# Kernel optimization log

Hardware: AMD Instinct MI355X
Metric: run time of the kernel (lower is better)

## Reference

```python
import jax, jax.numpy as jnp
import numpy as np

B, C, S, N, V = 8, 16, 512, 512, 128
EPS = 1e-5

def setup_inputs() -> dict:
    key = jax.random.key(0)
    ks = jax.random.split(key, 9)
    def u(k, shape, scale):
        return jax.random.uniform(k, shape, jnp.float32, -scale, scale)
    attn_scale = 12 * np.sqrt(3.0 / (S * N * V))      # custom attn_init for query / key.left / value2
    xav_vs = np.sqrt(6.0 / (V + S))                    # xavier_uniform for (C, V, S) or (C, S, V)
    xav_nv = np.sqrt(6.0 / (N + V))                    # xavier_uniform for (C, N, V)
    return {
        "x": jax.random.normal(ks[0], (B, C, S, N), jnp.float32),
        "wq": u(ks[1], (C, N, V), attn_scale),          # query weight (other_features=S)
        "k_left": u(ks[2], (C, V, S), attn_scale),      # key left (attn_init)
        "k_right": u(ks[3], (C, N, V), xav_nv),         # key right (xavier)
        "v1_left": u(ks[4], (C, V, S), xav_vs),         # value1 left (xavier, attn_init=False)
        "v1_right": u(ks[5], (C, N, V), attn_scale),    # value1 right (attn_init scale)
        "v2_w": u(ks[6], (C, V, S), attn_scale),        # value2 weight (other_features=N)
        "gamma": jnp.ones((C,), jnp.float32),
        "beta": jnp.zeros((C,), jnp.float32),
    }

def batch_scaler(y, gamma, beta):
    # normalize over dims (0, 2, 3); per-channel affine
    mean = jnp.mean(y, axis=(0, 2, 3), keepdims=True)
    var = jnp.mean(jnp.square(y - mean), axis=(0, 2, 3), keepdims=True)
    yhat = (y - mean) * jax.lax.rsqrt(var + EPS)
    return yhat * gamma[None, :, None, None] + beta[None, :, None, None]

def reference(x, wq, k_left, k_right, v1_left, v1_right, v2_w, gamma, beta):
    # x: [B,C,S,N]
    q = jnp.matmul(x, wq)                               # [B,C,S,V]
    k = jnp.matmul(jnp.matmul(k_left, x), k_right)       # (C,V,S)@x -> [B,C,V,N] @ (C,N,V) -> [B,C,V,V]
    attn = jax.nn.softmax(jnp.einsum('bcsv,bcwv->bcsw', q, k), axis=-1)  # q @ k^T, softmax last dim
    v1 = jnp.matmul(jnp.matmul(v1_left, x), v1_right)    # [B,C,V,V]
    v2 = jnp.matmul(v2_w, x)                             # [B,C,V,N]
    v = jnp.matmul(v1, v2)                               # [B,C,V,N]
    y = x + jnp.matmul(attn, v)                          # [B,C,S,N]
    return batch_scaler(y, gamma, beta)
```

## Files before the change

kernel.cpp:

```cpp
#include <hip/hip_runtime.h>
#include <math.h>


typedef short  bf16x8 __attribute__((ext_vector_type(8)));
typedef short  short8 __attribute__((ext_vector_type(8)));
typedef float  f32x4  __attribute__((ext_vector_type(4)));

__device__ __forceinline__ unsigned short f2bf(float f) {
    union { float f; unsigned u; } v; v.f = f;
    return (unsigned short)((v.u + 0x7FFF + ((v.u >> 16) & 1)) >> 16);
}
__device__ __forceinline__ float bf2f(unsigned short u) {
    union { unsigned u; float f; } v; v.u = (unsigned)u << 16; return v.f;
}

__device__ __forceinline__ void gload16(const void* g, void* l)
{
    __builtin_amdgcn_global_load_lds(
        (const __attribute__((address_space(1))) void*)g,
        (__attribute__((address_space(3))) void*)l, 16, 0, 0);
}

constexpr size_t OB_XB   = 0;
constexpr size_t OB_XT   = OB_XB  + 67108864;
constexpr size_t OB_KLB  = OB_XT  + 67108864;
constexpr size_t OB_V1LB = OB_KLB + 2097152;
constexpr size_t OB_V2WB = OB_V1LB+ 2097152;
constexpr size_t OB_WQT  = OB_V2WB+ 2097152;
constexpr size_t OB_KRT  = OB_WQT + 2097152;
constexpr size_t OB_V1RT = OB_KRT + 2097152;
constexpr size_t OB_BUF  = OB_V1RT+ 2097152;
constexpr size_t OB_V2T  = OB_BUF + 33554432;
constexpr size_t OB_KM   = OB_V2T + 16777216;
constexpr size_t OB_V1M  = OB_KM  + 4194304;
constexpr size_t OB_Q    = OB_V1M + 4194304;
constexpr size_t OB_ATT  = OB_Q   + 16777216;
constexpr size_t OB_VT   = OB_ATT + 16777216;
constexpr size_t OB_ST   = OB_VT  + 16777216;

template<int NSTEPS, int MF, int NF>
__device__ __forceinline__ void mmcore(const char* __restrict__ Ab, int ldaB,
                                       const char* __restrict__ Bb, int ldbB,
                                       f32x4 (&acc)[MF][NF],
                                       char* __restrict__ smA, char* __restrict__ smB,
                                       int wm, int wn)
{
    const int tid = threadIdx.x;
    const int w = tid >> 6, l = tid & 63, g = l >> 4, lr = l & 15;
    const int rl = l >> 3, ch = l & 7;

#pragma unroll 1
    for (int t = 0; t < NSTEPS; ++t) {
#pragma unroll
        for (int j = 0; j < 4; ++j) {
            const int row = w * 32 + j * 8 + rl;
            gload16(Ab + (size_t)row * ldaB + t * 128 + ((ch ^ (row & 7)) * 16),
                    smA + (w * 32 + j * 8) * 128);
        }
#pragma unroll
        for (int j = 0; j < 4; ++j) {
            const int row = w * 32 + j * 8 + rl;
            gload16(Bb + (size_t)row * ldbB + t * 128 + ((ch ^ (row & 7)) * 16),
                    smB + (w * 32 + j * 8) * 128);
        }
        __syncthreads();
#pragma unroll
        for (int ks = 0; ks < 2; ++ks) {
            bf16x8 av[MF], bv[NF];
            const int cc = ks * 4 + g;
#pragma unroll
            for (int i = 0; i < MF; ++i) { int rw = wm + i * 16 + lr;
                av[i] = *(const bf16x8*)(smA + rw * 128 + ((cc ^ (rw & 7)) * 16)); }
#pragma unroll
            for (int j = 0; j < NF; ++j) { int rw = wn + j * 16 + lr;
                bv[j] = *(const bf16x8*)(smB + rw * 128 + ((cc ^ (rw & 7)) * 16)); }
#pragma unroll
            for (int i = 0; i < MF; ++i)
#pragma unroll
                for (int j = 0; j < NF; ++j)
                    acc[i][j] = __builtin_amdgcn_mfma_f32_16x16x32_bf16(av[i], bv[j], acc[i][j], 0, 0, 0);
        }
        __syncthreads();
    }
}

__device__ __forceinline__ void epi_write_rm(const f32x4 (&acc)[4][4], char* sm)
{
    const int tid = threadIdx.x, w = tid >> 6, l = tid & 63, g = l >> 4, lr = l & 15;
    const int wm = (w >> 1) * 64, wn = (w & 1) * 64;
#pragma unroll
    for (int i = 0; i < 4; ++i)
#pragma unroll
        for (int j = 0; j < 4; ++j) {
            const int row = wm + i * 16 + g * 4, col = wn + j * 16 + lr;
#pragma unroll
            for (int r = 0; r < 4; ++r)
                *(unsigned short*)(sm + (row + r) * 272 + col * 2) = f2bf(acc[i][j][r]);
        }
}

__device__ __forceinline__ void epi_write_tr(const f32x4 (&acc)[4][4], char* sm)
{
    const int tid = threadIdx.x, w = tid >> 6, l = tid & 63, g = l >> 4, lr = l & 15;
    const int wm = (w >> 1) * 64, wn = (w & 1) * 64;
#pragma unroll
    for (int i = 0; i < 4; ++i)
#pragma unroll
        for (int j = 0; j < 4; ++j) {
            const int rv = wm + i * 16 + g * 4, cn = wn + j * 16 + lr;
            ushort4 pk = make_ushort4(f2bf(acc[i][j][0]), f2bf(acc[i][j][1]),
                                      f2bf(acc[i][j][2]), f2bf(acc[i][j][3]));
            *(ushort4*)(sm + cn * 272 + rv * 2) = pk;
        }
}

__device__ __forceinline__ void epi_flush(const char* sm, unsigned short* gout, int ldg)
{
    const int tid = threadIdx.x;
    const int r0 = tid >> 4, q = tid & 15;
#pragma unroll
    for (int rep = 0; rep < 8; ++rep) {
        const int row = rep * 16 + r0;
        *(short8*)((short*)gout + (size_t)row * ldg + q * 8) =
            *(const short8*)(sm + row * 272 + q * 16);
    }
    __syncthreads();
}

__global__ __launch_bounds__(256) void k_pre(const float* __restrict__ kl,
                                             const float* __restrict__ v1l,
                                             const float* __restrict__ v2w,
                                             unsigned short* __restrict__ klb,
                                             unsigned short* __restrict__ v1lb,
                                             unsigned short* __restrict__ v2wb,
                                             float* __restrict__ stats)
{
    if (blockIdx.x == 0 && blockIdx.y == 0 && threadIdx.x < 64) stats[threadIdx.x] = 0.f;
    const int sel = blockIdx.y;
    const float* src = sel == 0 ? kl : sel == 1 ? v1l : v2w;
    unsigned short* dst = sel == 0 ? klb : sel == 1 ? v1lb : v2wb;
    for (int i = blockIdx.x * 256 + threadIdx.x; i < 65536; i += gridDim.x * 256) {
        float4 v = ((const float4*)src)[i];
        ((ushort4*)dst)[i] = make_ushort4(f2bf(v.x), f2bf(v.y), f2bf(v.z), f2bf(v.w));
    }
}

__global__ __launch_bounds__(256) void ktransx(const float* __restrict__ x,
                                               unsigned short* __restrict__ xb,
                                               unsigned short* __restrict__ xt)
{
    __shared__ float tl[64][65];
    const int bc = blockIdx.z;
    const int r0 = blockIdx.y * 64, c0 = blockIdx.x * 64;
    const float* src = x + (size_t)bc * 262144;
    const int tid = threadIdx.x, rr = tid >> 4, cc = (tid & 15) * 4;
#pragma unroll
    for (int rep = 0; rep < 4; ++rep) {
        int row = rep * 16 + rr;
        float4 v = *(const float4*)(src + (size_t)(r0 + row) * 512 + c0 + cc);
        *(ushort4*)(xb + (size_t)bc * 262144 + (size_t)(r0 + row) * 512 + c0 + cc) =
            make_ushort4(f2bf(v.x), f2bf(v.y), f2bf(v.z), f2bf(v.w));
        tl[cc + 0][row] = v.x; tl[cc + 1][row] = v.y; tl[cc + 2][row] = v.z; tl[cc + 3][row] = v.w;
    }
    __syncthreads();
#pragma unroll
    for (int rep = 0; rep < 4; ++rep) {
        int crow = rep * 16 + rr;
        *(ushort4*)(xt + (size_t)bc * 262144 + (size_t)(c0 + crow) * 512 + r0 + cc) =
            make_ushort4(f2bf(tl[crow][cc]), f2bf(tl[crow][cc + 1]),
                         f2bf(tl[crow][cc + 2]), f2bf(tl[crow][cc + 3]));
    }
}

__global__ __launch_bounds__(256) void ktransw(const float* __restrict__ wq,
                                               const float* __restrict__ kr,
                                               const float* __restrict__ v1r,
                                               unsigned short* __restrict__ wqt,
                                               unsigned short* __restrict__ krt,
                                               unsigned short* __restrict__ v1rt)
{
    __shared__ float tl[64][65];
    const int p = blockIdx.z, widx = p >> 4, c = p & 15;
    const float* s = (widx == 0 ? wq : widx == 1 ? kr : v1r) + (size_t)c * 65536;
    unsigned short* d = (widx == 0 ? wqt : widx == 1 ? krt : v1rt) + (size_t)c * 65536;
    const int r0 = blockIdx.y * 64, c0 = blockIdx.x * 64;
    const int tid = threadIdx.x, rr = tid >> 4, cc = (tid & 15) * 4;
#pragma unroll
    for (int rep = 0; rep < 4; ++rep) {
        int row = rep * 16 + rr;
        float4 v = *(const float4*)(s + (size_t)(r0 + row) * 128 + c0 + cc);
        tl[cc + 0][row] = v.x; tl[cc + 1][row] = v.y; tl[cc + 2][row] = v.z; tl[cc + 3][row] = v.w;
    }
    __syncthreads();
#pragma unroll
    for (int rep = 0; rep < 4; ++rep) {
        int crow = rep * 16 + rr;
        *(ushort4*)(d + (size_t)(c0 + crow) * 512 + r0 + cc) =
            make_ushort4(f2bf(tl[crow][cc]), f2bf(tl[crow][cc + 1]),
                         f2bf(tl[crow][cc + 2]), f2bf(tl[crow][cc + 3]));
    }
}

__global__ __launch_bounds__(256, 2) void k_wx(const unsigned short* __restrict__ klb,
                                               const unsigned short* __restrict__ v1lb,
                                               const unsigned short* __restrict__ v2wb,
                                               const unsigned short* __restrict__ xt,
                                               unsigned short* __restrict__ bufb,
                                               unsigned short* __restrict__ v2t)
{
    __shared__ char smem[34816];
    char* smA = smem; char* smB = smem + 16384;
    const int mt = blockIdx.x >> 2, n0 = blockIdx.x & 3, bc = blockIdx.y, c = bc & 15;
    const unsigned short* W = mt == 0 ? klb : mt == 1 ? v1lb : v2wb;
    const char* Bb = (const char*)(xt + (size_t)bc * 262144 + (size_t)n0 * 65536);
    const int w = threadIdx.x >> 6;
    f32x4 acc[4][4] = {};
    mmcore<8, 4, 4>((const char*)(W + (size_t)c * 65536), 1024, Bb, 1024, acc, smA, smB,
                    (w >> 1) * 64, (w & 1) * 64);
    if (mt < 2) {
        epi_write_rm(acc, smem);
        __syncthreads();
        epi_flush(smem, bufb + (size_t)bc * 131072 + (size_t)mt * 65536 + n0 * 128, 512);
    } else {
        epi_write_tr(acc, smem);
        __syncthreads();
        epi_flush(smem, v2t + (size_t)bc * 65536 + (size_t)n0 * 16384, 128);
    }
}

__global__ __launch_bounds__(256, 2) void k_kr(const unsigned short* __restrict__ bufb,
                                               const unsigned short* __restrict__ krt,
                                               const unsigned short* __restrict__ v1rt,
                                               unsigned short* __restrict__ kmat,
                                               unsigned short* __restrict__ v1m)
{
    __shared__ char smem[34816];
    char* smA = smem; char* smB = smem + 16384;
    const int mt = blockIdx.x, bc = blockIdx.y, c = bc & 15;
    const int w = threadIdx.x >> 6;
    f32x4 acc[4][4] = {};
    mmcore<8, 4, 4>((const char*)(bufb + (size_t)bc * 131072 + (size_t)mt * 65536), 1024,
                    (const char*)((mt ? v1rt : krt) + (size_t)c * 65536), 1024, acc, smA, smB,
                    (w >> 1) * 64, (w & 1) * 64);
    epi_write_rm(acc, smem);
    __syncthreads();
    epi_flush(smem, (mt ? v1m : kmat) + (size_t)bc * 16384, 128);
}

__global__ __launch_bounds__(256, 2) void k_q(const unsigned short* __restrict__ xb,
                                              const unsigned short* __restrict__ wqt,
                                              unsigned short* __restrict__ q)
{
    __shared__ char smem[34816];
    char* smA = smem; char* smB = smem + 16384;
    const int mt = blockIdx.x, bc = blockIdx.y, c = bc & 15;
    const int w = threadIdx.x >> 6;
    f32x4 acc[4][4] = {};
    mmcore<8, 4, 4>((const char*)(xb + (size_t)bc * 262144 + (size_t)mt * 65536), 1024,
                    (const char*)(wqt + (size_t)c * 65536), 1024, acc, smA, smB,
                    (w >> 1) * 64, (w & 1) * 64);
    epi_write_rm(acc, smem);
    __syncthreads();
    epi_flush(smem, q + (size_t)bc * 65536 + (size_t)mt * 16384, 128);
}

__global__ __launch_bounds__(256, 2) void k_at(const unsigned short* __restrict__ q,
                                               const unsigned short* __restrict__ kmat,
                                               unsigned short* __restrict__ attn)
{
    __shared__ char smem[34816];
    char* smA = smem; char* smB = smem + 16384;
    const int mt = blockIdx.x, bc = blockIdx.y;
    const int tid = threadIdx.x, w = tid >> 6, l = tid & 63, g = l >> 4, lr = l & 15;
    f32x4 acc[2][8] = {};
    mmcore<2, 2, 8>((const char*)(q + (size_t)bc * 65536 + (size_t)mt * 16384), 256,
                    (const char*)(kmat + (size_t)bc * 16384), 256, acc, smA, smB,
                    w * 32, 0);
    char* wsl = smem + w * 8704;
    unsigned short* ob = attn + (size_t)bc * 65536 + (size_t)(mt * 128 + w * 32) * 128;
#pragma unroll
    for (int i = 0; i < 2; ++i)
#pragma unroll
        for (int r = 0; r < 4; ++r) {
            float mx = -3e38f;
#pragma unroll
            for (int fj = 0; fj < 8; ++fj) mx = fmaxf(mx, acc[i][fj][r]);
#pragma unroll
            for (int d = 1; d < 16; d <<= 1) mx = fmaxf(mx, __shfl_xor(mx, d));
            float s = 0.f, e[8];
#pragma unroll
            for (int fj = 0; fj < 8; ++fj) { e[fj] = __expf(acc[i][fj][r] - mx); s += e[fj]; }
#pragma unroll
            for (int d = 1; d < 16; d <<= 1) s += __shfl_xor(s, d);
            const float inv = 1.f / s;
            const int rowh = i * 16 + g * 4 + r;
#pragma unroll
            for (int fj = 0; fj < 8; ++fj)
                *(unsigned short*)(wsl + rowh * 272 + (fj * 16 + lr) * 2) = f2bf(e[fj] * inv);
        }
#pragma unroll
    for (int rep = 0; rep < 8; ++rep) {
        const int row = rep * 4 + (l >> 4);
        *(short8*)((short*)ob + (size_t)row * 128 + (l & 15) * 8) =
            *(const short8*)(wsl + row * 272 + (l & 15) * 16);
    }
}

__global__ __launch_bounds__(256, 2) void k_v(const unsigned short* __restrict__ v2t,
                                              const unsigned short* __restrict__ v1m,
                                              unsigned short* __restrict__ vt)
{
    __shared__ char smem[34816];
    char* smA = smem; char* smB = smem + 16384;
    const int mt = blockIdx.x, bc = blockIdx.y;
    const int w = threadIdx.x >> 6;
    f32x4 acc[4][4] = {};
    mmcore<2, 4, 4>((const char*)(v2t + (size_t)bc * 65536 + (size_t)mt * 16384), 256,
                    (const char*)(v1m + (size_t)bc * 16384), 256, acc, smA, smB,
                    (w >> 1) * 64, (w & 1) * 64);
    epi_write_rm(acc, smem);
    __syncthreads();
    epi_flush(smem, vt + (size_t)bc * 65536 + (size_t)mt * 16384, 128);
}

__global__ __launch_bounds__(256, 2) void k_y(const unsigned short* __restrict__ attn,
                                              const unsigned short* __restrict__ vt,
                                              const float* __restrict__ x,
                                              unsigned short* __restrict__ yb,
                                              float* __restrict__ stats)
{
    __shared__ char smem[34816];
    __shared__ float r1[4], r2[4];
    char* smA = smem; char* smB = smem + 16384;
    const int nx = blockIdx.x, my = blockIdx.y, bc = blockIdx.z, c = bc & 15;
    const int tid = threadIdx.x, w = tid >> 6, l = tid & 63, g = l >> 4, lr = l & 15;
    f32x4 acc[4][4] = {};
    mmcore<2, 4, 4>((const char*)(attn + (size_t)bc * 65536 + (size_t)my * 16384), 256,
                    (const char*)(vt + (size_t)bc * 65536 + (size_t)nx * 16384), 256, acc, smA, smB,
                    (w >> 1) * 64, (w & 1) * 64);
    const float* xw = x + (size_t)bc * 262144 + (size_t)my * 128 * 512 + nx * 128;
    const int wm = (w >> 1) * 64, wn = (w & 1) * 64;
    float lsum = 0.f, lss = 0.f;
#pragma unroll
    for (int i = 0; i < 4; ++i)
#pragma unroll
        for (int j = 0; j < 4; ++j)
#pragma unroll
            for (int r = 0; r < 4; ++r) {
                const int row = wm + i * 16 + g * 4 + r, col = wn + j * 16 + lr;
                const float yv = acc[i][j][r] + xw[(size_t)row * 512 + col];
                lsum += yv; lss += yv * yv;
                *(unsigned short*)(smem + row * 272 + col * 2) = f2bf(yv);
            }
#pragma unroll
    for (int d = 32; d >= 1; d >>= 1) { lsum += __shfl_xor(lsum, d); lss += __shfl_xor(lss, d); }
    if (l == 0) { r1[w] = lsum; r2[w] = lss; }
    __syncthreads();
    epi_flush(smem, yb + (size_t)bc * 262144 + (size_t)my * 128 * 512 + nx * 128, 512);
    if (tid == 0) {
        atomicAdd(&stats[c * 2 + 0], r1[0] + r1[1] + r1[2] + r1[3]);
        atomicAdd(&stats[c * 2 + 1], r2[0] + r2[1] + r2[2] + r2[3]);
    }
}

__global__ void k_fin(float* __restrict__ stats, const float* __restrict__ gamma,
                      const float* __restrict__ beta)
{
    const int c = threadIdx.x;
    if (c < 16) {
        const float cnt  = 2097152.f;
        const float mean = stats[c * 2 + 0] / cnt;
        const float var  = stats[c * 2 + 1] / cnt - mean * mean;
        const float sc   = rsqrtf(var + 1e-5f) * gamma[c];
        stats[32 + c * 2 + 0] = sc;
        stats[32 + c * 2 + 1] = beta[c] - mean * sc;
    }
}

__global__ __launch_bounds__(256) void k_norm(const unsigned short* __restrict__ yb,
                                              float* __restrict__ out,
                                              const float* __restrict__ stats)
{
    const int tot = 4194304;
    for (int i = blockIdx.x * 256 + threadIdx.x; i < tot; i += gridDim.x * 256) {
        const long e = (long)i * 8;
        const int c = (int)(e >> 18) & 15;
        const float sc = stats[32 + c * 2 + 0];
        const float sh = stats[32 + c * 2 + 1];
        short8 v = ((const short8*)yb)[i];
        float4 o0, o1;
        o0.x = bf2f((unsigned short)v[0]) * sc + sh;
        o0.y = bf2f((unsigned short)v[1]) * sc + sh;
        o0.z = bf2f((unsigned short)v[2]) * sc + sh;
        o0.w = bf2f((unsigned short)v[3]) * sc + sh;
        o1.x = bf2f((unsigned short)v[4]) * sc + sh;
        o1.y = bf2f((unsigned short)v[5]) * sc + sh;
        o1.z = bf2f((unsigned short)v[6]) * sc + sh;
        o1.w = bf2f((unsigned short)v[7]) * sc + sh;
        ((float4*)out)[(size_t)i * 2 + 0] = o0;
        ((float4*)out)[(size_t)i * 2 + 1] = o1;
    }
}

extern "C" void kernel_launch(void* const* d_in, const int* in_sizes, int n_in,
                              void* d_out, int out_size, void* d_ws, size_t ws_size,
                              hipStream_t stream)
{
    (void)in_sizes; (void)n_in; (void)out_size; (void)ws_size;
    const float* x     = (const float*)d_in[0];
    const float* wq    = (const float*)d_in[1];
    const float* kl    = (const float*)d_in[2];
    const float* kr    = (const float*)d_in[3];
    const float* v1l   = (const float*)d_in[4];
    const float* v1r   = (const float*)d_in[5];
    const float* v2w   = (const float*)d_in[6];
    const float* gamma = (const float*)d_in[7];
    const float* beta  = (const float*)d_in[8];
    float* out = (float*)d_out;
    char*  ws  = (char*)d_ws;

    unsigned short* xb   = (unsigned short*)(ws + OB_XB);
    unsigned short* yb   = xb;
    unsigned short* xt   = (unsigned short*)(ws + OB_XT);
    unsigned short* klb  = (unsigned short*)(ws + OB_KLB);
    unsigned short* v1lb = (unsigned short*)(ws + OB_V1LB);
    unsigned short* v2wb = (unsigned short*)(ws + OB_V2WB);
    unsigned short* wqt  = (unsigned short*)(ws + OB_WQT);
    unsigned short* krt  = (unsigned short*)(ws + OB_KRT);
    unsigned short* v1rt = (unsigned short*)(ws + OB_V1RT);
    unsigned short* bufb = (unsigned short*)(ws + OB_BUF);
    unsigned short* v2t  = (unsigned short*)(ws + OB_V2T);
    unsigned short* kmat = (unsigned short*)(ws + OB_KM);
    unsigned short* v1m  = (unsigned short*)(ws + OB_V1M);
    unsigned short* q    = (unsigned short*)(ws + OB_Q);
    unsigned short* attn = (unsigned short*)(ws + OB_ATT);
    unsigned short* vt   = (unsigned short*)(ws + OB_VT);
    float*          st   = (float*)(ws + OB_ST);

    hipLaunchKernelGGL(k_pre,   dim3(64, 3),     dim3(256), 0, stream, kl, v1l, v2w, klb, v1lb, v2wb, st);
    hipLaunchKernelGGL(ktransx, dim3(8, 8, 128), dim3(256), 0, stream, x, xb, xt);
    hipLaunchKernelGGL(ktransw, dim3(2, 8, 48),  dim3(256), 0, stream, wq, kr, v1r, wqt, krt, v1rt);
    hipLaunchKernelGGL(k_wx,    dim3(12, 128),   dim3(256), 0, stream, klb, v1lb, v2wb, xt, bufb, v2t);
    hipLaunchKernelGGL(k_kr,    dim3(2, 128),    dim3(256), 0, stream, bufb, krt, v1rt, kmat, v1m);
    hipLaunchKernelGGL(k_q,     dim3(4, 128),    dim3(256), 0, stream, xb, wqt, q);
    hipLaunchKernelGGL(k_at,    dim3(4, 128),    dim3(256), 0, stream, q, kmat, attn);
    hipLaunchKernelGGL(k_v,     dim3(4, 128),    dim3(256), 0, stream, v2t, v1m, vt);
    hipLaunchKernelGGL(k_y,     dim3(4, 4, 128), dim3(256), 0, stream, attn, vt, x, yb, st);
    hipLaunchKernelGGL(k_fin,   dim3(1), dim3(64), 0, stream, st, gamma, beta);
    hipLaunchKernelGGL(k_norm,  dim3(2048),      dim3(256), 0, stream, yb, out, st);
}
```

Before: 251.5 us.

## Fuse Q projection into attention-score kernel and merge small prep kernels

Q is no longer written to global memory. The k_qat kernel computes each 128-row Q tile with MFMA, stores it swizzled in LDS as bf16, and immediately multiplies it against the K matrix and applies the softmax. The weight bf16 conversion and transpose kernels are merged into one launch, and the stats finalize is folded into each k_norm block, which removes three launches in total. The cost is 64KB of LDS per block in k_qat, which may reduce occupancy below the declared 2 blocks per CU, and every norm block now redundantly recomputes the per-channel scale and shift.

```diff
diff --git a/kernel.cpp b/kernel.cpp
--- a/kernel.cpp
+++ b/kernel.cpp
@@ -33,8 +33,7 @@
 constexpr size_t OB_V2T  = OB_BUF + 33554432;
 constexpr size_t OB_KM   = OB_V2T + 16777216;
 constexpr size_t OB_V1M  = OB_KM  + 4194304;
-constexpr size_t OB_Q    = OB_V1M + 4194304;
-constexpr size_t OB_ATT  = OB_Q   + 16777216;
+constexpr size_t OB_ATT  = OB_V1M + 4194304;
 constexpr size_t OB_VT   = OB_ATT + 16777216;
 constexpr size_t OB_ST   = OB_VT  + 16777216;
 
@@ -127,21 +126,55 @@
     __syncthreads();
 }
 
-__global__ __launch_bounds__(256) void k_pre(const float* __restrict__ kl,
-                                             const float* __restrict__ v1l,
-                                             const float* __restrict__ v2w,
-                                             unsigned short* __restrict__ klb,
-                                             unsigned short* __restrict__ v1lb,
-                                             unsigned short* __restrict__ v2wb,
-                                             float* __restrict__ stats)
-{
-    if (blockIdx.x == 0 && blockIdx.y == 0 && threadIdx.x < 64) stats[threadIdx.x] = 0.f;
-    const int sel = blockIdx.y;
-    const float* src = sel == 0 ? kl : sel == 1 ? v1l : v2w;
-    unsigned short* dst = sel == 0 ? klb : sel == 1 ? v1lb : v2wb;
-    for (int i = blockIdx.x * 256 + threadIdx.x; i < 65536; i += gridDim.x * 256) {
-        float4 v = ((const float4*)src)[i];
-        ((ushort4*)dst)[i] = make_ushort4(f2bf(v.x), f2bf(v.y), f2bf(v.z), f2bf(v.w));
+__global__ __launch_bounds__(256) void k_prep(const float* __restrict__ kl,
+                                              const float* __restrict__ v1l,
+                                              const float* __restrict__ v2w,
+                                              const float* __restrict__ wq,
+                                              const float* __restrict__ kr,
+                                              const float* __restrict__ v1r,
+                                              unsigned short* __restrict__ klb,
+                                              unsigned short* __restrict__ v1lb,
+                                              unsigned short* __restrict__ v2wb,
+                                              unsigned short* __restrict__ wqt,
+                                              unsigned short* __restrict__ krt,
+                                              unsigned short* __restrict__ v1rt,
+                                              float* __restrict__ stats)
+{
+    __shared__ float tl[64][65];
+    const int id = blockIdx.x, tid = threadIdx.x;
+    if (id == 0 && tid < 64) stats[tid] = 0.f;
+    if (id < 192) {
+        const int sel = id >> 6, blk = id & 63;
+        const float* src = sel == 0 ? kl : sel == 1 ? v1l : v2w;
+        unsigned short* dst = sel == 0 ? klb : sel == 1 ? v1lb : v2wb;
+#pragma unroll
+        for (int r = 0; r < 4; ++r) {
+            const int i = blk * 1024 + r * 256 + tid;
+            float4 v = ((const float4*)src)[i];
+            ((ushort4*)dst)[i] = make_ushort4(f2bf(v.x), f2bf(v.y), f2bf(v.z), f2bf(v.w));
+        }
+        return;
+    }
+    const int id2 = id - 192;
+    const int p = id2 >> 4, rem = id2 & 15, by = rem >> 1, bx = rem & 1;
+    const int widx = p >> 4, c = p & 15;
+    const float* s = (widx == 0 ? wq : widx == 1 ? kr : v1r) + (size_t)c * 65536;
+    unsigned short* d = (widx == 0 ? wqt : widx == 1 ? krt : v1rt) + (size_t)c * 65536;
+    const int r0 = by * 64, c0 = bx * 64;
+    const int rr = tid >> 4, cc = (tid & 15) * 4;
+#pragma unroll
+    for (int rep = 0; rep < 4; ++rep) {
+        int row = rep * 16 + rr;
+        float4 v = *(const float4*)(s + (size_t)(r0 + row) * 128 + c0 + cc);
+        tl[cc + 0][row] = v.x; tl[cc + 1][row] = v.y; tl[cc + 2][row] = v.z; tl[cc + 3][row] = v.w;
+    }
+    __syncthreads();
+#pragma unroll
+    for (int rep = 0; rep < 4; ++rep) {
+        int crow = rep * 16 + rr;
+        *(ushort4*)(d + (size_t)(c0 + crow) * 512 + r0 + cc) =
+            make_ushort4(f2bf(tl[crow][cc]), f2bf(tl[crow][cc + 1]),
+                         f2bf(tl[crow][cc + 2]), f2bf(tl[crow][cc + 3]));
     }
 }
 
@@ -167,35 +200,6 @@
     for (int rep = 0; rep < 4; ++rep) {
         int crow = rep * 16 + rr;
         *(ushort4*)(xt + (size_t)bc * 262144 + (size_t)(c0 + crow) * 512 + r0 + cc) =
-            make_ushort4(f2bf(tl[crow][cc]), f2bf(tl[crow][cc + 1]),
-                         f2bf(tl[crow][cc + 2]), f2bf(tl[crow][cc + 3]));
-    }
-}
-
-__global__ __launch_bounds__(256) void ktransw(const float* __restrict__ wq,
-                                               const float* __restrict__ kr,
-                                               const float* __restrict__ v1r,
-                                               unsigned short* __restrict__ wqt,
-                                               unsigned short* __restrict__ krt,
-                                               unsigned short* __restrict__ v1rt)
-{
-    __shared__ float tl[64][65];
-    const int p = blockIdx.z, widx = p >> 4, c = p & 15;
-    const float* s = (widx == 0 ? wq : widx == 1 ? kr : v1r) + (size_t)c * 65536;
-    unsigned short* d = (widx == 0 ? wqt : widx == 1 ? krt : v1rt) + (size_t)c * 65536;
-    const int r0 = blockIdx.y * 64, c0 = blockIdx.x * 64;
-    const int tid = threadIdx.x, rr = tid >> 4, cc = (tid & 15) * 4;
-#pragma unroll
-    for (int rep = 0; rep < 4; ++rep) {
-        int row = rep * 16 + rr;
-        float4 v = *(const float4*)(s + (size_t)(r0 + row) * 128 + c0 + cc);
-        tl[cc + 0][row] = v.x; tl[cc + 1][row] = v.y; tl[cc + 2][row] = v.z; tl[cc + 3][row] = v.w;
-    }
-    __syncthreads();
-#pragma unroll
-    for (int rep = 0; rep < 4; ++rep) {
-        int crow = rep * 16 + rr;
-        *(ushort4*)(d + (size_t)(c0 + crow) * 512 + r0 + cc) =
             make_ushort4(f2bf(tl[crow][cc]), f2bf(tl[crow][cc + 1]),
                          f2bf(tl[crow][cc + 2]), f2bf(tl[crow][cc + 3]));
     }
@@ -247,35 +251,73 @@
     epi_flush(smem, (mt ? v1m : kmat) + (size_t)bc * 16384, 128);
 }
 
-__global__ __launch_bounds__(256, 2) void k_q(const unsigned short* __restrict__ xb,
-                                              const unsigned short* __restrict__ wqt,
-                                              unsigned short* __restrict__ q)
-{
-    __shared__ char smem[34816];
-    char* smA = smem; char* smB = smem + 16384;
+__global__ __launch_bounds__(256, 2) void k_qat(const unsigned short* __restrict__ xb,
+                                                const unsigned short* __restrict__ wqt,
+                                                const unsigned short* __restrict__ kmat,
+                                                unsigned short* __restrict__ attn)
+{
+    __shared__ char smem[65536];
+    char* smA = smem;
+    char* smB = smem + 16384;
+    char* qlds = smem + 32768;
     const int mt = blockIdx.x, bc = blockIdx.y, c = bc & 15;
-    const int w = threadIdx.x >> 6;
+    const int tid = threadIdx.x, w = tid >> 6, l = tid & 63, g = l >> 4, lr = l & 15;
+
     f32x4 acc[4][4] = {};
     mmcore<8, 4, 4>((const char*)(xb + (size_t)bc * 262144 + (size_t)mt * 65536), 1024,
                     (const char*)(wqt + (size_t)c * 65536), 1024, acc, smA, smB,
                     (w >> 1) * 64, (w & 1) * 64);
-    epi_write_rm(acc, smem);
-    __syncthreads();
-    epi_flush(smem, q + (size_t)bc * 65536 + (size_t)mt * 16384, 128);
-}
-
-__global__ __launch_bounds__(256, 2) void k_at(const unsigned short* __restrict__ q,
-                                               const unsigned short* __restrict__ kmat,
-                                               unsigned short* __restrict__ attn)
-{
-    __shared__ char smem[34816];
-    char* smA = smem; char* smB = smem + 16384;
-    const int mt = blockIdx.x, bc = blockIdx.y;
-    const int tid = threadIdx.x, w = tid >> 6, l = tid & 63, g = l >> 4, lr = l & 15;
-    f32x4 acc[2][8] = {};
-    mmcore<2, 2, 8>((const char*)(q + (size_t)bc * 65536 + (size_t)mt * 16384), 256,
-                    (const char*)(kmat + (size_t)bc * 16384), 256, acc, smA, smB,
-                    w * 32, 0);
+
+    {
+        const int wm = (w >> 1) * 64, wn = (w & 1) * 64;
+        const int t = wn >> 6;
+#pragma unroll
+        for (int i = 0; i < 4; ++i)
+#pragma unroll
+            for (int j = 0; j < 4; ++j) {
+                const int k6 = j * 16 + lr;
+                const int chunk = k6 >> 3, eb = (k6 & 7) << 1;
+#pragma unroll
+                for (int r = 0; r < 4; ++r) {
+                    const int row = wm + i * 16 + g * 4 + r;
+                    *(unsigned short*)(qlds + t * 16384 + row * 128 +
+                                       ((chunk ^ (row & 7)) << 4) + eb) = f2bf(acc[i][j][r]);
+                }
+            }
+    }
+    __syncthreads();
+
+    f32x4 acc2[2][8] = {};
+    const int rl = l >> 3, ch = l & 7;
+    const char* Kb = (const char*)(kmat + (size_t)bc * 16384);
+#pragma unroll
+    for (int t = 0; t < 2; ++t) {
+#pragma unroll
+        for (int j = 0; j < 4; ++j) {
+            const int row = w * 32 + j * 8 + rl;
+            gload16(Kb + (size_t)row * 256 + t * 128 + ((ch ^ (row & 7)) * 16),
+                    smB + (w * 32 + j * 8) * 128);
+        }
+        __syncthreads();
+#pragma unroll
+        for (int ks = 0; ks < 2; ++ks) {
+            const int cc2 = ks * 4 + g;
+            bf16x8 av[2], bv[8];
+#pragma unroll
+            for (int i = 0; i < 2; ++i) { const int rw = w * 32 + i * 16 + lr;
+                av[i] = *(const bf16x8*)(qlds + t * 16384 + rw * 128 + ((cc2 ^ (rw & 7)) * 16)); }
+#pragma unroll
+            for (int j = 0; j < 8; ++j) { const int rw = j * 16 + lr;
+                bv[j] = *(const bf16x8*)(smB + rw * 128 + ((cc2 ^ (rw & 7)) * 16)); }
+#pragma unroll
+            for (int i = 0; i < 2; ++i)
+#pragma unroll
+                for (int j = 0; j < 8; ++j)
+                    acc2[i][j] = __builtin_amdgcn_mfma_f32_16x16x32_bf16(av[i], bv[j], acc2[i][j], 0, 0, 0);
+        }
+        __syncthreads();
+    }
+
     char* wsl = smem + w * 8704;
     unsigned short* ob = attn + (size_t)bc * 65536 + (size_t)(mt * 128 + w * 32) * 128;
 #pragma unroll
@@ -284,12 +326,12 @@
         for (int r = 0; r < 4; ++r) {
             float mx = -3e38f;
 #pragma unroll
-            for (int fj = 0; fj < 8; ++fj) mx = fmaxf(mx, acc[i][fj][r]);
+            for (int fj = 0; fj < 8; ++fj) mx = fmaxf(mx, acc2[i][fj][r]);
 #pragma unroll
             for (int d = 1; d < 16; d <<= 1) mx = fmaxf(mx, __shfl_xor(mx, d));
             float s = 0.f, e[8];
 #pragma unroll
-            for (int fj = 0; fj < 8; ++fj) { e[fj] = __expf(acc[i][fj][r] - mx); s += e[fj]; }
+            for (int fj = 0; fj < 8; ++fj) { e[fj] = __expf(acc2[i][fj][r] - mx); s += e[fj]; }
 #pragma unroll
             for (int d = 1; d < 16; d <<= 1) s += __shfl_xor(s, d);
             const float inv = 1.f / s;
@@ -363,30 +405,29 @@
     }
 }
 
-__global__ void k_fin(float* __restrict__ stats, const float* __restrict__ gamma,
-                      const float* __restrict__ beta)
-{
-    const int c = threadIdx.x;
-    if (c < 16) {
+__global__ __launch_bounds__(256) void k_norm(const unsigned short* __restrict__ yb,
+                                              float* __restrict__ out,
+                                              const float* __restrict__ stats,
+                                              const float* __restrict__ gamma,
+                                              const float* __restrict__ beta)
+{
+    __shared__ float ssc[16], ssh[16];
+    if (threadIdx.x < 16) {
+        const int c = threadIdx.x;
         const float cnt  = 2097152.f;
         const float mean = stats[c * 2 + 0] / cnt;
         const float var  = stats[c * 2 + 1] / cnt - mean * mean;
         const float sc   = rsqrtf(var + 1e-5f) * gamma[c];
-        stats[32 + c * 2 + 0] = sc;
-        stats[32 + c * 2 + 1] = beta[c] - mean * sc;
-    }
-}
-
-__global__ __launch_bounds__(256) void k_norm(const unsigned short* __restrict__ yb,
-                                              float* __restrict__ out,
-                                              const float* __restrict__ stats)
-{
+        ssc[c] = sc;
+        ssh[c] = beta[c] - mean * sc;
+    }
+    __syncthreads();
     const int tot = 4194304;
     for (int i = blockIdx.x * 256 + threadIdx.x; i < tot; i += gridDim.x * 256) {
         const long e = (long)i * 8;
         const int c = (int)(e >> 18) & 15;
-        const float sc = stats[32 + c * 2 + 0];
-        const float sh = stats[32 + c * 2 + 1];
+        const float sc = ssc[c];
+        const float sh = ssh[c];
         short8 v = ((const short8*)yb)[i];
         float4 o0, o1;
         o0.x = bf2f((unsigned short)v[0]) * sc + sh;
@@ -432,20 +473,17 @@
     unsigned short* v2t  = (unsigned short*)(ws + OB_V2T);
     unsigned short* kmat = (unsigned short*)(ws + OB_KM);
     unsigned short* v1m  = (unsigned short*)(ws + OB_V1M);
-    unsigned short* q    = (unsigned short*)(ws + OB_Q);
     unsigned short* attn = (unsigned short*)(ws + OB_ATT);
     unsigned short* vt   = (unsigned short*)(ws + OB_VT);
     float*          st   = (float*)(ws + OB_ST);
 
-    hipLaunchKernelGGL(k_pre,   dim3(64, 3),     dim3(256), 0, stream, kl, v1l, v2w, klb, v1lb, v2wb, st);
+    hipLaunchKernelGGL(k_prep,  dim3(960),       dim3(256), 0, stream,
+                       kl, v1l, v2w, wq, kr, v1r, klb, v1lb, v2wb, wqt, krt, v1rt, st);
     hipLaunchKernelGGL(ktransx, dim3(8, 8, 128), dim3(256), 0, stream, x, xb, xt);
-    hipLaunchKernelGGL(ktransw, dim3(2, 8, 48),  dim3(256), 0, stream, wq, kr, v1r, wqt, krt, v1rt);
     hipLaunchKernelGGL(k_wx,    dim3(12, 128),   dim3(256), 0, stream, klb, v1lb, v2wb, xt, bufb, v2t);
     hipLaunchKernelGGL(k_kr,    dim3(2, 128),    dim3(256), 0, stream, bufb, krt, v1rt, kmat, v1m);
-    hipLaunchKernelGGL(k_q,     dim3(4, 128),    dim3(256), 0, stream, xb, wqt, q);
-    hipLaunchKernelGGL(k_at,    dim3(4, 128),    dim3(256), 0, stream, q, kmat, attn);
+    hipLaunchKernelGGL(k_qat,   dim3(4, 128),    dim3(256), 0, stream, xb, wqt, kmat, attn);
     hipLaunchKernelGGL(k_v,     dim3(4, 128),    dim3(256), 0, stream, v2t, v1m, vt);
     hipLaunchKernelGGL(k_y,     dim3(4, 4, 128), dim3(256), 0, stream, attn, vt, x, yb, st);
-    hipLaunchKernelGGL(k_fin,   dim3(1), dim3(64), 0, stream, st, gamma, beta);
-    hipLaunchKernelGGL(k_norm,  dim3(2048),      dim3(256), 0, stream, yb, out, st);
-}
+    hipLaunchKernelGGL(k_norm,  dim3(2048),      dim3(256), 0, stream, yb, out, st, gamma, beta);
+}
```

Measured after the change: 241.8 us. -3.9%, faster.
